# Optimization experiments

Hardware: AMD Instinct MI355X
Metric: run time of the kernel (lower is better)

Reference implementation:

```python
import jax, jax.numpy as jnp
import numpy as np

D_MODEL = 1024
N_HEADS = 16
N_KV_HEADS = 4
D_K = D_MODEL // N_HEADS
Q_SIZE = D_MODEL
KV_SIZE = N_KV_HEADS * D_K
QKV_SIZE = Q_SIZE + 2 * KV_SIZE
EPS = 1.1920929e-07  # torch.nn.RMSNorm default eps (fp32 machine eps)
ROPE_BASE = 10000.0


def rms_norm(x, w):
    # normalize over last dim, learned scale (torch nn.RMSNorm)
    return x * jax.lax.rsqrt(jnp.mean(x * x, axis=-1, keepdims=True) + EPS) * w


def rope(x):
    # torchtune RotaryPositionalEmbeddings: interleaved pairs, x is [B,T,H,D]
    T, d = x.shape[1], x.shape[-1]
    inv_freq = 1.0 / (ROPE_BASE ** (jnp.arange(0, d, 2, dtype=jnp.float32) / d))
    ang = jnp.arange(T, dtype=jnp.float32)[:, None] * inv_freq[None, :]  # [T, d/2]
    cos = jnp.cos(ang)[None, :, None, :]
    sin = jnp.sin(ang)[None, :, None, :]
    xr = x.reshape(x.shape[:-1] + (d // 2, 2))
    x1, x2 = xr[..., 0], xr[..., 1]
    out = jnp.stack([x1 * cos - x2 * sin, x1 * sin + x2 * cos], axis=-1)
    return out.reshape(x.shape)


def setup_inputs() -> dict:
    key = jax.random.key(0)
    k1, k2 = jax.random.split(key)
    x = jax.random.normal(k1, (2, 2048, D_MODEL), dtype=jnp.float32)
    qkvo = jax.random.normal(k2, (QKV_SIZE + D_MODEL, D_MODEL), dtype=jnp.float32) * 0.02
    q_norm_w = jnp.ones((D_K,), dtype=jnp.float32)
    k_norm_w = jnp.ones((D_K,), dtype=jnp.float32)
    return {"x": x, "qkvo": qkvo, "q_norm_w": q_norm_w, "k_norm_w": k_norm_w}


def reference(x, qkvo, q_norm_w, k_norm_w):
    B, T, _ = x.shape
    groups = N_HEADS // N_KV_HEADS
    qkv = x @ qkvo[:QKV_SIZE].T  # [B,T,qkv_size]
    Q = qkv[..., :Q_SIZE].reshape(B, T, N_HEADS, D_K)
    K = qkv[..., Q_SIZE:Q_SIZE + KV_SIZE].reshape(B, T, N_KV_HEADS, D_K)
    V = qkv[..., Q_SIZE + KV_SIZE:].reshape(B, T, N_KV_HEADS, D_K)
    Q = rope(rms_norm(Q, q_norm_w))
    K = rope(rms_norm(K, k_norm_w))
    K = jnp.repeat(K, groups, axis=2)  # GQA expand to [B,T,H,D]
    V = jnp.repeat(V, groups, axis=2)
    scale = 1.0 / np.sqrt(D_K).astype(np.float32)
    scores = jnp.einsum('bqhd,bkhd->bhqk', Q, K) * scale
    causal = jnp.tril(jnp.ones((T, T), dtype=bool))
    scores = jnp.where(causal[None, None], scores, jnp.float32(-jnp.inf))
    attn = jax.nn.softmax(scores, axis=-1)
    out = jnp.einsum('bhqk,bkhd->bqhd', attn, V).reshape(B, T, D_MODEL)
    return out @ qkvo[QKV_SIZE:].T
```

## Files before the change

kernel.cpp:

```cpp
#include <hip/hip_runtime.h>
#include <hip/hip_bf16.h>
#include <cstdint>
#include <cstddef>

typedef __bf16 bf16x8 __attribute__((ext_vector_type(8)));
typedef float f32x4 __attribute__((ext_vector_type(4)));

__device__ __forceinline__ unsigned short f2bf(float f) {
    unsigned u = __builtin_bit_cast(unsigned, f);
    u += 0x7FFFu + ((u >> 16) & 1u);
    return (unsigned short)(u >> 16);
}
__device__ __forceinline__ unsigned pk2(float a, float b) {
    typedef __bf16 bf16x2 __attribute__((ext_vector_type(2)));
    bf16x2 h;
    h[0] = (__bf16)a;
    h[1] = (__bf16)b;
    unsigned r;
    __builtin_memcpy(&r, &h, 4);
    return r;
}
__device__ __forceinline__ float fexp2(float x) {
#if __has_builtin(__builtin_amdgcn_exp2f)
    return __builtin_amdgcn_exp2f(x);
#else
    return __expf(x * 0.6931471805599453f);
#endif
}
__device__ __forceinline__ void gld16(const void* g, void* l) {
    __builtin_amdgcn_global_load_lds((const __attribute__((address_space(1))) void*)g,
                                     (__attribute__((address_space(3))) void*)l, 16, 0, 0);
}

__global__ __launch_bounds__(256) void cast_kernel(const float4* __restrict__ x,
                                                   const float4* __restrict__ w,
                                                   ushort4* __restrict__ xbf,
                                                   ushort4* __restrict__ wbf,
                                                   float2* __restrict__ tab) {
    int i = blockIdx.x * 256 + threadIdx.x;
    const int NX4 = 4096 * 1024 / 4;
    const int NW4 = 2560 * 1024 / 4;
    if (i < NX4 + NW4) {
        float4 v;
        ushort4* o;
        if (i < NX4) { v = x[i]; o = xbf + i; }
        else { v = w[i - NX4]; o = wbf + (i - NX4); }
        ushort4 r;
        r.x = f2bf(v.x); r.y = f2bf(v.y); r.z = f2bf(v.z); r.w = f2bf(v.w);
        *o = r;
    } else {
        int k = i - NX4 - NW4;
        if (k >= 2048 * 32) return;
        int t = k >> 5, fp = k & 31;
        float inv = __expf(-(float)(2 * fp) * (1.0f / 64.0f) * 9.210340371976184f);
        float sn, cs;
        sincosf((float)t * inv, &sn, &cs);
        tab[k] = make_float2(cs, sn);
    }
}

__global__ __launch_bounds__(256) void gemm_qkv_fused(const ushort* __restrict__ A,
                                                      const ushort* __restrict__ B,
                                                      const float2* __restrict__ tab,
                                                      const float* __restrict__ qw,
                                                      const float* __restrict__ kw,
                                                      ushort* __restrict__ Qo,
                                                      ushort* __restrict__ Ko,
                                                      ushort* __restrict__ VT) {
    const int K = 1024;
    __shared__ __align__(16) ushort LA[2][4096];
    __shared__ __align__(16) ushort LB[2][8192];
    int tid = threadIdx.x;
    int w = tid >> 6, lane = tid & 63;
    int qm = lane & 15, quad = lane >> 4;

    int nbx = gridDim.x, nby = gridDim.y;
    int nwg = nbx * nby;
    int f = blockIdx.y * nbx + blockIdx.x;
    int q = nwg >> 3, r = nwg & 7;
    int xcd = f & 7, idx = f >> 3;
    int s = (xcd < r ? xcd * (q + 1) : r * (q + 1) + (xcd - r) * q) + idx;
    int m0 = (s / nby) * 64;
    int n0 = (s % nby) * 128;

    int mw = (w & 1) * 32, nw = (w >> 1) * 64;
    int sw = qm & 7;

    f32x4 acc[2][4];
#pragma unroll
    for (int i = 0; i < 2; i++)
#pragma unroll
        for (int j = 0; j < 4; j++) acc[i][j] = (f32x4){0.f, 0.f, 0.f, 0.f};

    int sa[2], ra[2], ga[2];
#pragma unroll
    for (int u = 0; u < 2; u++) {
        sa[u] = tid + u * 256;
        ra[u] = sa[u] >> 3;
        ga[u] = (sa[u] & 7) ^ (ra[u] & 7);
    }
    int sb[4], rb[4], gb[4];
#pragma unroll
    for (int u = 0; u < 4; u++) {
        sb[u] = tid + u * 256;
        rb[u] = sb[u] >> 3;
        gb[u] = (sb[u] & 7) ^ (rb[u] & 7);
    }

    auto do_stage = [&](int k0, int buf) {
#pragma unroll
        for (int u = 0; u < 2; u++)
            gld16(A + (size_t)(m0 + ra[u]) * K + k0 + ga[u] * 8, &LA[buf][sa[u] * 8]);
#pragma unroll
        for (int u = 0; u < 4; u++)
            gld16(B + (size_t)(n0 + rb[u]) * K + k0 + gb[u] * 8, &LB[buf][sb[u] * 8]);
    };

    do_stage(0, 0);
    int buf = 0;
    for (int k0 = 0; k0 < K; k0 += 64, buf ^= 1) {
        __syncthreads();
        if (k0 + 64 < K) do_stage(k0 + 64, buf ^ 1);
        bf16x8 a[2][2], bb[4][2];
#pragma unroll
        for (int mi = 0; mi < 2; mi++)
#pragma unroll
            for (int h = 0; h < 2; h++)
                a[mi][h] = *(const bf16x8*)&LA[buf][((mw + mi * 16 + qm) * 8 + ((h * 4 + quad) ^ sw)) * 8];
#pragma unroll
        for (int ni = 0; ni < 4; ni++)
#pragma unroll
            for (int h = 0; h < 2; h++)
                bb[ni][h] = *(const bf16x8*)&LB[buf][((nw + ni * 16 + qm) * 8 + ((h * 4 + quad) ^ sw)) * 8];
#pragma unroll
        for (int h = 0; h < 2; h++)
#pragma unroll
            for (int mi = 0; mi < 2; mi++)
#pragma unroll
                for (int ni = 0; ni < 4; ni++)
                    acc[mi][ni] = __builtin_amdgcn_mfma_f32_16x16x32_bf16(a[mi][h], bb[ni][h], acc[mi][ni], 0, 0, 0);
    }

    int head_col0 = n0 + nw;
    int rowbase = m0 + mw;
    int b = rowbase >> 11;
    int t0g = rowbase & 2047;
    bool isV = (head_col0 >= 1280);

    __syncthreads();
    if (isV) {
        ushort* lv = &LA[0][0] + w * 2048;
#pragma unroll
        for (int mi = 0; mi < 2; mi++)
#pragma unroll
            for (int r2 = 0; r2 < 4; r2++) {
                int tt = mi * 16 + quad * 4 + r2;
                int pcl = ((tt >> 2) & 3) * 8 + ((tt >> 4) & 1) * 4 + (tt & 3);
#pragma unroll
                for (int ni = 0; ni < 4; ni++)
                    lv[(ni * 16 + qm) * 32 + pcl] = f2bf(acc[mi][ni][r2]);
            }
    } else {
        bool isQ = (head_col0 < 1024);
        const float* wp = isQ ? qw : kw;
        float wt[4];
#pragma unroll
        for (int ni = 0; ni < 4; ni++) wt[ni] = wp[ni * 16 + qm];
        float qs = isQ ? 0.18033688011112042f : 1.0f;
        ushort* op = isQ ? (Qo + (size_t)(b * 16 + (head_col0 >> 6)) * 2048 * 64)
                         : (Ko + (size_t)(b * 4 + ((head_col0 - 1024) >> 6)) * 2048 * 64);
#pragma unroll
        for (int mi = 0; mi < 2; mi++)
#pragma unroll
            for (int r2 = 0; r2 < 4; r2++) {
                float ssum = acc[mi][0][r2] * acc[mi][0][r2] + acc[mi][1][r2] * acc[mi][1][r2]
                           + acc[mi][2][r2] * acc[mi][2][r2] + acc[mi][3][r2] * acc[mi][3][r2];
                ssum += __shfl_xor(ssum, 1);
                ssum += __shfl_xor(ssum, 2);
                ssum += __shfl_xor(ssum, 4);
                ssum += __shfl_xor(ssum, 8);
                float rinv = rsqrtf(ssum * (1.0f / 64.0f) + 1.1920929e-7f);
                int t = t0g + mi * 16 + quad * 4 + r2;
#pragma unroll
                for (int ni = 0; ni < 4; ni++) {
                    float vn = acc[mi][ni][r2] * rinv * wt[ni];
                    float2 cssn = tab[t * 32 + ni * 8 + (qm >> 1)];
                    float pr = __shfl_xor(vn, 1);
                    float out = (qm & 1) ? fmaf(pr, cssn.y, vn * cssn.x)
                                         : fmaf(vn, cssn.x, -pr * cssn.y);
                    op[(size_t)t * 64 + ni * 16 + qm] = f2bf(out * qs);
                }
            }
    }
    __syncthreads();
    if (isV) {
        const ushort* lv = &LA[0][0] + w * 2048;
        int vh = (head_col0 - 1280) >> 6;
        int bkv = b * 4 + vh;
#pragma unroll
        for (int j = 0; j < 8; j++) {
            int d = j * 8 + (lane >> 3);
            uint2 v = *(const uint2*)&lv[d * 32 + (lane & 7) * 4];
            *(uint2*)&VT[((size_t)(bkv * 64 + d)) * 2048 + t0g + (lane & 7) * 4] = v;
        }
    }
}

__global__ __launch_bounds__(256) void gemm_bf16(const ushort* __restrict__ A,
                                                 const ushort* __restrict__ B,
                                                 float* __restrict__ C,
                                                 int M, int N, int K) {
    __shared__ __align__(16) ushort LA[2][4096];
    __shared__ __align__(16) ushort LB[2][8192];
    int tid = threadIdx.x;
    int w = tid >> 6, lane = tid & 63;
    int qm = lane & 15, quad = lane >> 4;

    int nbx = gridDim.x, nby = gridDim.y;
    int nwg = nbx * nby;
    int f = blockIdx.y * nbx + blockIdx.x;
    int q = nwg >> 3, r = nwg & 7;
    int xcd = f & 7, idx = f >> 3;
    int s = (xcd < r ? xcd * (q + 1) : r * (q + 1) + (xcd - r) * q) + idx;
    int m0 = (s / nby) * 64;
    int n0 = (s % nby) * 128;

    int mw = (w & 1) * 32, nw = (w >> 1) * 64;
    int sw = qm & 7;

    f32x4 acc[2][4];
#pragma unroll
    for (int i = 0; i < 2; i++)
#pragma unroll
        for (int j = 0; j < 4; j++) acc[i][j] = (f32x4){0.f, 0.f, 0.f, 0.f};

    int sa[2], ra[2], ga[2];
#pragma unroll
    for (int u = 0; u < 2; u++) {
        sa[u] = tid + u * 256;
        ra[u] = sa[u] >> 3;
        ga[u] = (sa[u] & 7) ^ (ra[u] & 7);
    }
    int sb[4], rb[4], gb[4];
#pragma unroll
    for (int u = 0; u < 4; u++) {
        sb[u] = tid + u * 256;
        rb[u] = sb[u] >> 3;
        gb[u] = (sb[u] & 7) ^ (rb[u] & 7);
    }

    auto do_stage = [&](int k0, int buf) {
#pragma unroll
        for (int u = 0; u < 2; u++)
            gld16(A + (size_t)(m0 + ra[u]) * K + k0 + ga[u] * 8, &LA[buf][sa[u] * 8]);
#pragma unroll
        for (int u = 0; u < 4; u++)
            gld16(B + (size_t)(n0 + rb[u]) * K + k0 + gb[u] * 8, &LB[buf][sb[u] * 8]);
    };

    do_stage(0, 0);
    int buf = 0;
    for (int k0 = 0; k0 < K; k0 += 64, buf ^= 1) {
        __syncthreads();
        if (k0 + 64 < K) do_stage(k0 + 64, buf ^ 1);
        bf16x8 a[2][2], bb[4][2];
#pragma unroll
        for (int mi = 0; mi < 2; mi++)
#pragma unroll
            for (int h = 0; h < 2; h++)
                a[mi][h] = *(const bf16x8*)&LA[buf][((mw + mi * 16 + qm) * 8 + ((h * 4 + quad) ^ sw)) * 8];
#pragma unroll
        for (int ni = 0; ni < 4; ni++)
#pragma unroll
            for (int h = 0; h < 2; h++)
                bb[ni][h] = *(const bf16x8*)&LB[buf][((nw + ni * 16 + qm) * 8 + ((h * 4 + quad) ^ sw)) * 8];
#pragma unroll
        for (int h = 0; h < 2; h++)
#pragma unroll
            for (int mi = 0; mi < 2; mi++)
#pragma unroll
                for (int ni = 0; ni < 4; ni++)
                    acc[mi][ni] = __builtin_amdgcn_mfma_f32_16x16x32_bf16(a[mi][h], bb[ni][h], acc[mi][ni], 0, 0, 0);
    }
#pragma unroll
    for (int mi = 0; mi < 2; mi++)
#pragma unroll
        for (int ni = 0; ni < 4; ni++) {
            int row = m0 + mw + mi * 16 + quad * 4;
            int col = n0 + nw + ni * 16 + qm;
            float* cp = C + (size_t)row * N + col;
#pragma unroll
            for (int r2 = 0; r2 < 4; r2++) cp[(size_t)r2 * N] = acc[mi][ni][r2];
        }
}

__global__ __launch_bounds__(256) void attn14_kernel(const ushort* __restrict__ Q,
                                                     const ushort* __restrict__ K,
                                                     const ushort* __restrict__ VT,
                                                     ushort* __restrict__ O) {
    __shared__ __align__(16) ushort KT[2][8192];
    __shared__ __align__(16) ushort VL[2][8192];

    int blk = blockIdx.x;
    int qp = 31 - (blk >> 5);
    int bh = blk & 31;
    int tid = threadIdx.x;
    int w = tid >> 6, lane = tid & 63;
    int qm = lane & 15, quad = lane >> 4;
    int b = bh >> 4, h = bh & 15;
    int bkv = b * 4 + (h >> 2);

    const ushort* Qbh = Q + (size_t)bh * 2048 * 64;
    const ushort* Kbh = K + (size_t)bkv * 2048 * 64;
    const ushort* Vbh = VT + (size_t)bkv * 64 * 2048;
    int sw = qm & 7;

    int sk[4], rk[4], gk[4], sv[4], rv[4], gv[4];
#pragma unroll
    for (int u = 0; u < 4; u++) {
        sk[u] = tid + u * 256;
        rk[u] = sk[u] >> 3;
        gk[u] = (sk[u] & 7) ^ (rk[u] & 7);
        sv[u] = tid + u * 256;
        rv[u] = sv[u] >> 4;
        gv[u] = (sv[u] & 15) ^ (rv[u] & 7);
    }

    auto do_stage = [&](int j0, int buf) {
#pragma unroll
        for (int u = 0; u < 4; u++)
            gld16(Kbh + (size_t)(j0 + rk[u]) * 64 + gk[u] * 8, &KT[buf][sk[u] * 8]);
#pragma unroll
        for (int u = 0; u < 4; u++)
            gld16(Vbh + (size_t)rv[u] * 2048 + j0 + gv[u] * 8, &VL[buf][sv[u] * 8]);
    };

    int nch = (qp + 2) >> 1;
    int q0 = qp * 64 + w * 16;
    const ushort* qptr = Qbh + (size_t)(q0 + qm) * 64 + quad * 8;
    bf16x8 qb0 = *(const bf16x8*)qptr;
    bf16x8 qb1 = *(const bf16x8*)(qptr + 32);
    f32x4 oacc[4];
    float lacc = 0.f;
#pragma unroll
    for (int i = 0; i < 4; i++) oacc[i] = (f32x4){0.f, 0.f, 0.f, 0.f};

    do_stage(0, 0);
    int buf = 0;
#pragma unroll 1
    for (int i = 0; i < nch; i++, buf ^= 1) {
        int j0 = i * 128;
        __syncthreads();
        if (i + 1 < nch) do_stage(j0 + 128, buf ^ 1);

        f32x4 st[8];
#pragma unroll
        for (int tj = 0; tj < 8; tj++) st[tj] = (f32x4){0.f, 0.f, 0.f, 0.f};
#pragma unroll
        for (int tj = 0; tj < 8; tj++) {
            bf16x8 kf0 = *(const bf16x8*)&KT[buf][((16 * tj + qm) * 8 + (quad ^ sw)) * 8];
            bf16x8 kf1 = *(const bf16x8*)&KT[buf][((16 * tj + qm) * 8 + ((4 + quad) ^ sw)) * 8];
            st[tj] = __builtin_amdgcn_mfma_f32_16x16x32_bf16(kf0, qb0, st[tj], 0, 0, 0);
            st[tj] = __builtin_amdgcn_mfma_f32_16x16x32_bf16(kf1, qb1, st[tj], 0, 0, 0);
        }
        if (i == nch - 1) {
#pragma unroll
            for (int tj = 0; tj < 8; tj++)
#pragma unroll
                for (int r = 0; r < 4; r++) {
                    int key = j0 + tj * 16 + quad * 4 + r;
                    if (key > q0 + qm) st[tj][r] = -1e30f;
                }
        }
        float rs = 0.f;
#pragma unroll
        for (int tj = 0; tj < 8; tj++)
#pragma unroll
            for (int r = 0; r < 4; r++) {
                float pv = fexp2(st[tj][r]);
                st[tj][r] = pv;
                rs += pv;
            }
        lacc += rs;

        bf16x8 pf[4];
#pragma unroll
        for (int ks = 0; ks < 4; ks++) {
            unsigned up[4];
            up[0] = pk2(st[2 * ks][0], st[2 * ks][1]);
            up[1] = pk2(st[2 * ks][2], st[2 * ks][3]);
            up[2] = pk2(st[2 * ks + 1][0], st[2 * ks + 1][1]);
            up[3] = pk2(st[2 * ks + 1][2], st[2 * ks + 1][3]);
            __builtin_memcpy(&pf[ks], up, 16);
        }

#pragma unroll
        for (int dt = 0; dt < 4; dt++) {
            int base = (16 * dt + qm) * 16;
#pragma unroll
            for (int ks = 0; ks < 4; ks++) {
                bf16x8 vf = *(const bf16x8*)&VL[buf][(base + ((ks * 4 + quad) ^ sw)) * 8];
                oacc[dt] = __builtin_amdgcn_mfma_f32_16x16x32_bf16(vf, pf[ks], oacc[dt], 0, 0, 0);
            }
        }
    }
    float l = lacc;
    l += __shfl_xor(l, 16);
    l += __shfl_xor(l, 32);
    float rinv = 1.0f / l;
    uint2 val;
#pragma unroll
    for (int dt = 0; dt < 4; dt++) {
        val.x = pk2(oacc[dt][0] * rinv, oacc[dt][1] * rinv);
        val.y = pk2(oacc[dt][2] * rinv, oacc[dt][3] * rinv);
        *(uint2*)&O[((size_t)(b * 2048) + q0 + qm) * 1024 + h * 64 + dt * 16 + quad * 4] = val;
    }
}

extern "C" void kernel_launch(void* const* d_in, const int* in_sizes, int n_in,
                              void* d_out, int out_size, void* d_ws, size_t ws_size,
                              hipStream_t stream) {
    (void)in_sizes; (void)n_in; (void)out_size; (void)ws_size;
    const float* x    = (const float*)d_in[0];
    const float* qkvo = (const float*)d_in[1];
    const float* qw   = (const float*)d_in[2];
    const float* kw   = (const float*)d_in[3];
    float* out = (float*)d_out;

    char* ws = (char*)d_ws;
    ushort* xbf = (ushort*)(ws + 0);
    ushort* wbf = (ushort*)(ws + 8388608);
    float2* tab = (float2*)(ws + 13631488);
    ushort* Qb  = (ushort*)(ws + 38797312);
    ushort* Kb  = (ushort*)(ws + 47185920);
    ushort* VT  = (ushort*)(ws + 49283072);
    ushort* Ob  = (ushort*)(ws + 51380224);

    cast_kernel<<<6912, 256, 0, stream>>>((const float4*)x, (const float4*)qkvo,
                                          (ushort4*)xbf, (ushort4*)wbf, tab);
    gemm_qkv_fused<<<dim3(64, 12), 256, 0, stream>>>(xbf, wbf, tab, qw, kw, Qb, Kb, VT);
    attn14_kernel<<<1024, 256, 0, stream>>>(Qb, Kb, VT, Ob);
    gemm_bf16<<<dim3(64, 8), 256, 0, stream>>>(Ob, wbf + (size_t)1536 * 1024, out, 4096, 1024, 1024);
}
```

Baseline: 148.0 us.

## Process two GQA query heads per attention block to share K/V tiles

Each attention block now handles two query heads that share the same KV head. Every K/V tile staged into shared memory feeds both heads' QK and PV MFMAs, which halves global K/V traffic and staging per unit of work. The grid shrinks from 1024 to 512 blocks. In exchange, per-thread register pressure roughly doubles for the accumulators, which may lower occupancy, and there are fewer blocks to balance the uneven causal workload.

```diff
diff --git a/kernel.cpp b/kernel.cpp
--- a/kernel.cpp
+++ b/kernel.cpp
@@ -294,7 +294,7 @@
         }
 }
 
-__global__ __launch_bounds__(256) void attn14_kernel(const ushort* __restrict__ Q,
+__global__ __launch_bounds__(256) void attn15_kernel(const ushort* __restrict__ Q,
                                                      const ushort* __restrict__ K,
                                                      const ushort* __restrict__ VT,
                                                      ushort* __restrict__ O) {
@@ -302,15 +302,18 @@
     __shared__ __align__(16) ushort VL[2][8192];
 
     int blk = blockIdx.x;
-    int qp = 31 - (blk >> 5);
-    int bh = blk & 31;
+    int qp = 31 - (blk >> 4);
+    int low4 = blk & 15;
+    int b = low4 >> 3;
+    int kvh = (low4 >> 1) & 3;
+    int hp = low4 & 1;
+    int h0 = kvh * 4 + hp * 2;
+    int bkv = b * 4 + kvh;
     int tid = threadIdx.x;
     int w = tid >> 6, lane = tid & 63;
     int qm = lane & 15, quad = lane >> 4;
-    int b = bh >> 4, h = bh & 15;
-    int bkv = b * 4 + (h >> 2);
-
-    const ushort* Qbh = Q + (size_t)bh * 2048 * 64;
+
+    const ushort* Qb0 = Q + (size_t)(b * 16 + h0) * 2048 * 64;
     const ushort* Kbh = K + (size_t)bkv * 2048 * 64;
     const ushort* Vbh = VT + (size_t)bkv * 64 * 2048;
     int sw = qm & 7;
@@ -337,13 +340,19 @@
 
     int nch = (qp + 2) >> 1;
     int q0 = qp * 64 + w * 16;
-    const ushort* qptr = Qbh + (size_t)(q0 + qm) * 64 + quad * 8;
-    bf16x8 qb0 = *(const bf16x8*)qptr;
-    bf16x8 qb1 = *(const bf16x8*)(qptr + 32);
-    f32x4 oacc[4];
-    float lacc = 0.f;
-#pragma unroll
-    for (int i = 0; i < 4; i++) oacc[i] = (f32x4){0.f, 0.f, 0.f, 0.f};
+    bf16x8 qb[2][2];
+#pragma unroll
+    for (int hh = 0; hh < 2; hh++) {
+        const ushort* qptr = Qb0 + (size_t)hh * 2048 * 64 + (size_t)(q0 + qm) * 64 + quad * 8;
+        qb[hh][0] = *(const bf16x8*)qptr;
+        qb[hh][1] = *(const bf16x8*)(qptr + 32);
+    }
+    f32x4 oacc[2][4];
+    float lacc[2] = {0.f, 0.f};
+#pragma unroll
+    for (int hh = 0; hh < 2; hh++)
+#pragma unroll
+        for (int i = 0; i < 4; i++) oacc[hh][i] = (f32x4){0.f, 0.f, 0.f, 0.f};
 
     do_stage(0, 0);
     int buf = 0;
@@ -353,67 +362,73 @@
         __syncthreads();
         if (i + 1 < nch) do_stage(j0 + 128, buf ^ 1);
 
-        f32x4 st[8];
-#pragma unroll
-        for (int tj = 0; tj < 8; tj++) st[tj] = (f32x4){0.f, 0.f, 0.f, 0.f};
-#pragma unroll
-        for (int tj = 0; tj < 8; tj++) {
-            bf16x8 kf0 = *(const bf16x8*)&KT[buf][((16 * tj + qm) * 8 + (quad ^ sw)) * 8];
-            bf16x8 kf1 = *(const bf16x8*)&KT[buf][((16 * tj + qm) * 8 + ((4 + quad) ^ sw)) * 8];
-            st[tj] = __builtin_amdgcn_mfma_f32_16x16x32_bf16(kf0, qb0, st[tj], 0, 0, 0);
-            st[tj] = __builtin_amdgcn_mfma_f32_16x16x32_bf16(kf1, qb1, st[tj], 0, 0, 0);
+#pragma unroll
+        for (int hh = 0; hh < 2; hh++) {
+            f32x4 st[8];
+#pragma unroll
+            for (int tj = 0; tj < 8; tj++) st[tj] = (f32x4){0.f, 0.f, 0.f, 0.f};
+#pragma unroll
+            for (int tj = 0; tj < 8; tj++) {
+                bf16x8 kf0 = *(const bf16x8*)&KT[buf][((16 * tj + qm) * 8 + (quad ^ sw)) * 8];
+                bf16x8 kf1 = *(const bf16x8*)&KT[buf][((16 * tj + qm) * 8 + ((4 + quad) ^ sw)) * 8];
+                st[tj] = __builtin_amdgcn_mfma_f32_16x16x32_bf16(kf0, qb[hh][0], st[tj], 0, 0, 0);
+                st[tj] = __builtin_amdgcn_mfma_f32_16x16x32_bf16(kf1, qb[hh][1], st[tj], 0, 0, 0);
+            }
+            if (i == nch - 1) {
+#pragma unroll
+                for (int tj = 0; tj < 8; tj++)
+#pragma unroll
+                    for (int r = 0; r < 4; r++) {
+                        int key = j0 + tj * 16 + quad * 4 + r;
+                        if (key > q0 + qm) st[tj][r] = -1e30f;
+                    }
+            }
+            float rs = 0.f;
+#pragma unroll
+            for (int tj = 0; tj < 8; tj++)
+#pragma unroll
+                for (int r = 0; r < 4; r++) {
+                    float pv = fexp2(st[tj][r]);
+                    st[tj][r] = pv;
+                    rs += pv;
+                }
+            lacc[hh] += rs;
+
+            bf16x8 pf[4];
+#pragma unroll
+            for (int ks = 0; ks < 4; ks++) {
+                unsigned up[4];
+                up[0] = pk2(st[2 * ks][0], st[2 * ks][1]);
+                up[1] = pk2(st[2 * ks][2], st[2 * ks][3]);
+                up[2] = pk2(st[2 * ks + 1][0], st[2 * ks + 1][1]);
+                up[3] = pk2(st[2 * ks + 1][2], st[2 * ks + 1][3]);
+                __builtin_memcpy(&pf[ks], up, 16);
+            }
+
+#pragma unroll
+            for (int dt = 0; dt < 4; dt++) {
+                int base = (16 * dt + qm) * 16;
+#pragma unroll
+                for (int ks = 0; ks < 4; ks++) {
+                    bf16x8 vf = *(const bf16x8*)&VL[buf][(base + ((ks * 4 + quad) ^ sw)) * 8];
+                    oacc[hh][dt] = __builtin_amdgcn_mfma_f32_16x16x32_bf16(vf, pf[ks], oacc[hh][dt], 0, 0, 0);
+                }
+            }
         }
-        if (i == nch - 1) {
-#pragma unroll
-            for (int tj = 0; tj < 8; tj++)
-#pragma unroll
-                for (int r = 0; r < 4; r++) {
-                    int key = j0 + tj * 16 + quad * 4 + r;
-                    if (key > q0 + qm) st[tj][r] = -1e30f;
-                }
+    }
+#pragma unroll
+    for (int hh = 0; hh < 2; hh++) {
+        float l = lacc[hh];
+        l += __shfl_xor(l, 16);
+        l += __shfl_xor(l, 32);
+        float rinv = 1.0f / l;
+        uint2 val;
+#pragma unroll
+        for (int dt = 0; dt < 4; dt++) {
+            val.x = pk2(oacc[hh][dt][0] * rinv, oacc[hh][dt][1] * rinv);
+            val.y = pk2(oacc[hh][dt][2] * rinv, oacc[hh][dt][3] * rinv);
+            *(uint2*)&O[((size_t)(b * 2048) + q0 + qm) * 1024 + (h0 + hh) * 64 + dt * 16 + quad * 4] = val;
         }
-        float rs = 0.f;
-#pragma unroll
-        for (int tj = 0; tj < 8; tj++)
-#pragma unroll
-            for (int r = 0; r < 4; r++) {
-                float pv = fexp2(st[tj][r]);
-                st[tj][r] = pv;
-                rs += pv;
-            }
-        lacc += rs;
-
-        bf16x8 pf[4];
-#pragma unroll
-        for (int ks = 0; ks < 4; ks++) {
-            unsigned up[4];
-            up[0] = pk2(st[2 * ks][0], st[2 * ks][1]);
-            up[1] = pk2(st[2 * ks][2], st[2 * ks][3]);
-            up[2] = pk2(st[2 * ks + 1][0], st[2 * ks + 1][1]);
-            up[3] = pk2(st[2 * ks + 1][2], st[2 * ks + 1][3]);
-            __builtin_memcpy(&pf[ks], up, 16);
-        }
-
-#pragma unroll
-        for (int dt = 0; dt < 4; dt++) {
-            int base = (16 * dt + qm) * 16;
-#pragma unroll
-            for (int ks = 0; ks < 4; ks++) {
-                bf16x8 vf = *(const bf16x8*)&VL[buf][(base + ((ks * 4 + quad) ^ sw)) * 8];
-                oacc[dt] = __builtin_amdgcn_mfma_f32_16x16x32_bf16(vf, pf[ks], oacc[dt], 0, 0, 0);
-            }
-        }
-    }
-    float l = lacc;
-    l += __shfl_xor(l, 16);
-    l += __shfl_xor(l, 32);
-    float rinv = 1.0f / l;
-    uint2 val;
-#pragma unroll
-    for (int dt = 0; dt < 4; dt++) {
-        val.x = pk2(oacc[dt][0] * rinv, oacc[dt][1] * rinv);
-        val.y = pk2(oacc[dt][2] * rinv, oacc[dt][3] * rinv);
-        *(uint2*)&O[((size_t)(b * 2048) + q0 + qm) * 1024 + h * 64 + dt * 16 + quad * 4] = val;
     }
 }
 
@@ -439,6 +454,6 @@
     cast_kernel<<<6912, 256, 0, stream>>>((const float4*)x, (const float4*)qkvo,
                                           (ushort4*)xbf, (ushort4*)wbf, tab);
     gemm_qkv_fused<<<dim3(64, 12), 256, 0, stream>>>(xbf, wbf, tab, qw, kw, Qb, Kb, VT);
-    attn14_kernel<<<1024, 256, 0, stream>>>(Qb, Kb, VT, Ob);
+    attn15_kernel<<<512, 256, 0, stream>>>(Qb, Kb, VT, Ob);
     gemm_bf16<<<dim3(64, 8), 256, 0, stream>>>(Ob, wbf + (size_t)1536 * 1024, out, 4096, 1024, 1024);
 }
```

New measurement: 157.4 us. 6.3% more time.
